# Kernel optimization log

Hardware: AMD Instinct MI355X
Metric: run time of the kernel (lower is better)

## Reference

```python
import jax, jax.numpy as jnp
import numpy as np

BS, V, S, K = 4, 2048, 7, 10
CLASS_NUM, VEC_NUM, CAT = 6, 8, 16
OUT_HEAD = CLASS_NUM + VEC_NUM * 3  # 30
DIM_FUSE = 128 + 128 + 256 + 256 + 512 + 512 + 16  # 1808


def _normalize(x, axis):
    return x / jnp.maximum(jnp.linalg.norm(x, axis=axis, keepdims=True), 1e-12)


def knn_index(verts, k):
    # verts: (b, v, 3) -> (b, v, k) excluding self
    inner = jnp.einsum('bnd,bmd->bnm', verts, verts)
    sq = jnp.sum(verts * verts, axis=2)
    dist = sq[:, :, None] + sq[:, None, :] - 2.0 * inner
    _, idx = jax.lax.top_k(-dist, k + 1)
    return idx[:, :, 1:]


def nearest_index(target, source):
    # target: (b, v1, 3), source: (b, v2, 3) -> (b, v1)
    inner = jnp.einsum('bnd,bmd->bnm', target, source)
    d = jnp.sum(source * source, 2)[:, None, :] + jnp.sum(target * target, 2)[:, :, None] - 2.0 * inner
    return jnp.argmin(d, axis=-1)


def gather_nb(t, idx):
    # t: (b, v, d), idx: (b, v1, k) -> (b, v1, k, d)
    return jax.vmap(lambda tt, ii: tt[ii])(t, idx)


def gather1(t, idx):
    # t: (b, v, d), idx: (b, v1) -> (b, v1, d)
    return jax.vmap(lambda tt, ii: tt[ii])(t, idx)


def bn_train(x, g, b, eps=1e-5):
    # x: (b, v, c); BatchNorm1d training-mode over (batch, vertices)
    m = jnp.mean(x, axis=(0, 1), keepdims=True)
    v = jnp.var(x, axis=(0, 1), keepdims=True)
    return (x - m) * jax.lax.rsqrt(v + eps) * g + b


def conv_surface(nb_idx, verts, directions, s, kernel_num):
    nd = _normalize(gather_nb(verts, nb_idx) - verts[:, :, None, :], -1)  # (b,v,n,3)
    sd = _normalize(directions, 0)  # (3, s*k)
    theta = jax.nn.relu(jnp.einsum('bvnd,dk->bvnk', nd, sd))
    b_, v_, n_, _ = theta.shape
    theta = theta.reshape(b_, v_, n_, s, kernel_num)
    return jnp.sum(jnp.max(theta, axis=2), axis=2)  # (b, v, kernel_num)


def conv_layer(nb_idx, verts, fm, w, b, directions, s, out_ch):
    nd = _normalize(gather_nb(verts, nb_idx) - verts[:, :, None, :], -1)
    sd = _normalize(directions, 0)  # (3, s*out_ch)
    theta = jax.nn.relu(jnp.einsum('bvnd,dk->bvnk', nd, sd))  # (b,v,n,s*o)
    fo = jnp.einsum('bvc,ck->bvk', fm, w) + b  # (b, v, (s+1)*o)
    center = fo[..., :out_ch]
    supp = gather_nb(fo[..., out_ch:], nb_idx)  # (b,v,n,s*o)
    act = (theta * supp).reshape(theta.shape[0], theta.shape[1], theta.shape[2], s, out_ch)
    act = jnp.sum(jnp.max(act, axis=2), axis=2)  # (b, v, o)
    return center + act


def pool_layer(verts, fm, pooling_rate, nb_num):
    idx = knn_index(verts, nb_num)
    pooled = jnp.max(gather_nb(fm, idx), axis=2)
    pool_num = verts.shape[1] // pooling_rate
    # deterministic subsample (torch uses randperm; fixed arange for reproducibility)
    return verts[:, :pool_num], pooled[:, :pool_num]


def setup_inputs() -> dict:
    key = jax.random.key(0)
    ks = jax.random.split(key, 16)
    def rn(i, shape, scale=0.05):
        return jax.random.normal(ks[i], shape, dtype=jnp.float32) * scale
    z = lambda *s: jnp.zeros(s, jnp.float32)
    o = lambda *s: jnp.ones(s, jnp.float32)
    return {
        'vertices': jax.random.normal(ks[0], (BS, V, 3), dtype=jnp.float32),
        'onehot': jax.nn.one_hot(jax.random.randint(ks[1], (BS,), 0, CAT), CAT, dtype=jnp.float32),
        'dir0': rn(2, (3, S * 128)),
        'w1': rn(3, (128, (S + 1) * 128)), 'b1': z((S + 1) * 128), 'dir1': rn(4, (3, S * 128)),
        'w2': rn(5, (128, (S + 1) * 256)), 'b2': z((S + 1) * 256), 'dir2': rn(6, (3, S * 256)),
        'w3': rn(7, (256, (S + 1) * 256)), 'b3': z((S + 1) * 256), 'dir3': rn(8, (3, S * 256)),
        'w4': rn(9, (256, (S + 1) * 512)), 'b4': z((S + 1) * 512), 'dir4': rn(10, (3, S * 512)),
        'g_bn1': o(128), 'be_bn1': z(128),
        'g_bn2': o(256), 'be_bn2': z(256),
        'g_bn3': o(256), 'be_bn3': z(256),
        'wc1': rn(11, (512, DIM_FUSE)), 'bc1': z(512),
        'wc2': rn(12, (512, 512)), 'bc2': z(512),
        'wc3': rn(13, (OUT_HEAD, 512)), 'bc3': z(OUT_HEAD),
    }


def reference(vertices, onehot, dir0, w1, b1, dir1, w2, b2, dir2, w3, b3, dir3,
              w4, b4, dir4, g_bn1, be_bn1, g_bn2, be_bn2, g_bn3, be_bn3,
              wc1, bc1, wc2, bc2, wc3, bc3):
    bs, v_num, _ = vertices.shape
    nb = knn_index(vertices, K)
    fm0 = jax.nn.relu(conv_surface(nb, vertices, dir0, S, 128))
    fm1 = jax.nn.relu(bn_train(conv_layer(nb, vertices, fm0, w1, b1, dir1, S, 128), g_bn1, be_bn1))
    vp1, fp1 = pool_layer(vertices, fm1, 4, 4)
    nb1 = knn_index(vp1, min(K, vp1.shape[1] // 8))
    fm2 = jax.nn.relu(bn_train(conv_layer(nb1, vp1, fp1, w2, b2, dir2, S, 256), g_bn2, be_bn2))
    fm3 = jax.nn.relu(bn_train(conv_layer(nb1, vp1, fm2, w3, b3, dir3, S, 256), g_bn3, be_bn3))
    vp2, fp2 = pool_layer(vp1, fm3, 4, 4)
    nb2 = knn_index(vp2, min(K, vp2.shape[1] // 8))
    fm4 = conv_layer(nb2, vp2, fp2, w4, b4, dir4, S, 512)
    f_global = jnp.max(fm4, axis=1)  # (b, 512)
    n1 = nearest_index(vertices, vp1)
    n2 = nearest_index(vertices, vp2)
    fm2u = gather1(fm2, n1)
    fm3u = gather1(fm3, n1)
    fm4u = gather1(fm4, n2)
    fg = jnp.broadcast_to(f_global[:, None, :], (bs, v_num, 512))
    oh = jnp.broadcast_to(onehot[:, None, :], (bs, v_num, CAT))
    feat = jnp.concatenate([fm0, fm1, fm2u, fm3u, fm4u, oh], axis=2)
    fuse = jnp.concatenate([fm0, fm1, fm2u, fm3u, fm4u, fg, oh], axis=2)
    h = jax.nn.relu(jnp.einsum('bvc,oc->bvo', fuse, wc1) + bc1)
    h = jax.nn.relu(jnp.einsum('bvc,oc->bvo', h, wc2) + bc2)
    pred = jnp.einsum('bvc,oc->bvo', h, wc3) + bc3
    seg = pred[..., :CLASS_NUM]
    vecs = pred[..., CLASS_NUM:CLASS_NUM + VEC_NUM * 3]
    return (seg, vecs, feat)
```

## Files before the change

kernel.cpp:

```cpp
#include <hip/hip_runtime.h>
#include <hip/hip_bf16.h>
#include <math.h>

#define BSZ 4
#define VN 2048
#define SS 7
#define KNB 10

typedef __attribute__((ext_vector_type(8))) short short8;
typedef __attribute__((ext_vector_type(4))) float f32x4;
typedef __attribute__((address_space(1))) const void gcvoid;
typedef __attribute__((address_space(3))) void lvoid;

__device__ inline ushort f2bf(float x) {
    __hip_bfloat16 h = __float2bfloat16(x);
    return *(ushort*)&h;
}

__device__ inline void gl2lds16(const ushort* g, ushort* l) {
    __builtin_amdgcn_global_load_lds((gcvoid*)g, (lvoid*)l, 16, 0, 0);
}

__device__ inline unsigned fenc(float f) {
    unsigned b = __float_as_uint(f);
    return (b & 0x80000000u) ? ~b : (b | 0x80000000u);
}
__device__ inline float fdec(unsigned e) {
    unsigned b = (e & 0x80000000u) ? (e & 0x7FFFFFFFu) : ~e;
    return __uint_as_float(b);
}

#define INS(dq, iq, dd, jj) { bool lt_ = (dd) < (dq); \
    float dmn_ = lt_ ? (dd) : (dq); float dmx_ = lt_ ? (dq) : (dd); \
    int imn_ = lt_ ? (jj) : (iq); int imx_ = lt_ ? (iq) : (jj); \
    (dq) = dmn_; (iq) = imn_; (dd) = dmx_; (jj) = imx_; }

#define PB0 8960L
#define PB1 24320L
#define PB2 958208L
#define PB3 1220352L

__global__ void prep_uber(const float* __restrict__ d0, const float* __restrict__ d1,
                          const float* __restrict__ d2, const float* __restrict__ d3,
                          const float* __restrict__ d4,
                          float* __restrict__ s0, float* __restrict__ s1,
                          float* __restrict__ s2, float* __restrict__ s3, float* __restrict__ s4,
                          const float* __restrict__ wc3, float* __restrict__ wc3t,
                          const float* __restrict__ wc1, ushort* __restrict__ wc1b,
                          const float* __restrict__ wc2, ushort* __restrict__ wc2b) {
    long i = blockIdx.x * 256L + threadIdx.x;
    if (i < PB0) {
        const float* src; float* dst; int C, c;
        if (i < 896)        { src = d0; dst = s0; C = 896;  c = (int)i; }
        else if (i < 1792)  { src = d1; dst = s1; C = 896;  c = (int)i - 896; }
        else if (i < 3584)  { src = d2; dst = s2; C = 1792; c = (int)i - 1792; }
        else if (i < 5376)  { src = d3; dst = s3; C = 1792; c = (int)i - 3584; }
        else                { src = d4; dst = s4; C = 3584; c = (int)i - 5376; }
        float a = src[c], b = src[C + c], e = src[2 * C + c];
        float den = fmaxf(sqrtf(a * a + b * b + e * e), 1e-12f);
        dst[c] = a / den; dst[C + c] = b / den; dst[2 * C + c] = e / den;
    } else if (i < PB1) {
        long j = i - PB0;
        int o = (int)(j / 512), k = (int)(j % 512);
        wc3t[(long)k * 30 + o] = wc3[j];
    } else if (i < PB2) {
        long j = i - PB1;
        int c = (int)(j % 1824);
        long r = j / 1824;
        wc1b[j] = f2bf(c < 1808 ? wc1[r * 1808 + c] : 0.f);
    } else if (i < PB3) {
        long j = i - PB2;
        wc2b[j] = f2bf(wc2[j]);
    }
}

__global__ __launch_bounds__(256) void wt_trans_all(const float* __restrict__ w1, const float* __restrict__ w2,
                                                    const float* __restrict__ w3, const float* __restrict__ w4,
                                                    ushort* __restrict__ o1, ushort* __restrict__ o2,
                                                    ushort* __restrict__ o3, ushort* __restrict__ o4) {
    __shared__ float tile[32][33];
    int gb = blockIdx.x;
    const float* w; ushort* o; int K, N, t;
    if (gb < 128)      { w = w1; o = o1; K = 128; N = 1024; t = gb; }
    else if (gb < 384) { w = w2; o = o2; K = 128; N = 2048; t = gb - 128; }
    else if (gb < 896) { w = w3; o = o3; K = 256; N = 2048; t = gb - 384; }
    else               { w = w4; o = o4; K = 256; N = 4096; t = gb - 896; }
    int tn = t % (N / 32), tk = t / (N / 32);
    int n0 = tn * 32, k0 = tk * 32;
    int tx = threadIdx.x % 32, ty = threadIdx.x / 32;
#pragma unroll
    for (int r = 0; r < 32; r += 8)
        tile[ty + r][tx] = w[(long)(k0 + ty + r) * N + n0 + tx];
    __syncthreads();
#pragma unroll
    for (int r = 0; r < 32; r += 8)
        o[(long)(n0 + ty + r) * K + k0 + tx] = f2bf(tile[tx][ty + r]);
}

#define KOFF0 0L
#define KOFF1 2621440L
#define KOFF2 2785280L
#define KTOT  2795520L

__device__ void knn_part_dev(const float* __restrict__ verts, int T, int nch,
                             int tile, int b, int ch,
                             float* __restrict__ pd, int* __restrict__ pi,
                             float4* __restrict__ s4) {
    const float* vb = verts + (long)b * VN * 3;
    int j0 = ch * 128;
    for (int j = threadIdx.x; j < 128; j += 128) {
        float x = vb[(j0 + j) * 3 + 0];
        float y = vb[(j0 + j) * 3 + 1];
        float z = vb[(j0 + j) * 3 + 2];
        s4[j] = make_float4(x, y, z, x * x + y * y + z * z);
    }
    __syncthreads();
    int i = tile * 128 + (int)threadIdx.x;
    if (i >= T) return;
    float px = vb[i * 3], py = vb[i * 3 + 1], pz = vb[i * 3 + 2];
    float d0[10], d1[10]; int id0[10], id1[10];
#pragma unroll
    for (int q = 0; q < 10; q++) { d0[q] = 1e30f; id0[q] = 0; d1[q] = 1e30f; id1[q] = 0; }
    for (int j = 0; j < 64; j++) {
        float4 sA = s4[j];
        float4 sB = s4[64 + j];
        float dA = fmaf(-2.f, px * sA.x + py * sA.y + pz * sA.z, sA.w);
        float dB = fmaf(-2.f, px * sB.x + py * sB.y + pz * sB.z, sB.w);
        int jA = j0 + j, jB = j0 + 64 + j;
        dA = (jA == i) ? 1e30f : dA;
        dB = (jB == i) ? 1e30f : dB;
#pragma unroll
        for (int q = 0; q < 10; q++) { INS(d0[q], id0[q], dA, jA); }
#pragma unroll
        for (int q = 0; q < 10; q++) { INS(d1[q], id1[q], dB, jB); }
    }
    long base = (((long)b * T + i) * nch * 2 + 2 * ch) * 10;
#pragma unroll
    for (int q = 0; q < 10; q++) { pd[base + q] = d0[q]; pi[base + q] = id0[q]; }
#pragma unroll
    for (int q = 0; q < 10; q++) { pd[base + 10 + q] = d1[q]; pi[base + 10 + q] = id1[q]; }
}

__device__ void nearest_dev(const float* __restrict__ verts, int SN, int* __restrict__ out,
                            int gl, float4* __restrict__ s4) {
    int t = gl * 128 + (int)threadIdx.x;
    int b = t / VN;
    const float* vb = verts + (long)b * VN * 3;
    for (int j = threadIdx.x; j < SN; j += 128) {
        float x = vb[j * 3], y = vb[j * 3 + 1], z = vb[j * 3 + 2];
        s4[j] = make_float4(x, y, z, x * x + y * y + z * z);
    }
    __syncthreads();
    int i = t % VN;
    float px = vb[i * 3], py = vb[i * 3 + 1], pz = vb[i * 3 + 2];
    int h = SN / 2;
    float b0 = 1e30f, b1 = 1e30f; int i0 = 0, i1 = 0;
    for (int j = 0; j < h; j++) {
        float4 sA = s4[j];
        float4 sB = s4[h + j];
        float dA = fmaf(-2.f, px * sA.x + py * sA.y + pz * sA.z, sA.w);
        float dB = fmaf(-2.f, px * sB.x + py * sB.y + pz * sB.z, sB.w);
        bool lA = dA < b0; b0 = lA ? dA : b0; i0 = lA ? j : i0;
        bool lB = dB < b1; b1 = lB ? dB : b1; i1 = lB ? (h + j) : i1;
    }
    out[t] = (b1 < b0) ? i1 : i0;
}

__global__ __launch_bounds__(128) void knn_part_uber(const float* __restrict__ verts,
                                                     float* __restrict__ pd, int* __restrict__ pi,
                                                     int* __restrict__ n1, int* __restrict__ n2) {
    __shared__ float4 smem[512];
    int gb = blockIdx.x;
    if (gb < 1024) {
        int tile = gb & 15, bc = gb >> 4;
        knn_part_dev(verts, 2048, 16, tile, bc >> 4, bc & 15, pd + KOFF0, pi + KOFF0, smem);
    } else if (gb < 1088) {
        int local = gb - 1024;
        int tile = local & 3, bc = local >> 2;
        knn_part_dev(verts, 512, 4, tile, bc >> 2, bc & 3, pd + KOFF1, pi + KOFF1, smem);
    } else if (gb < 1092) {
        int local = gb - 1088;
        knn_part_dev(verts, 128, 1, 0, local, 0, pd + KOFF2, pi + KOFF2, smem);
    } else if (gb < 1156) {
        nearest_dev(verts, 512, n1, gb - 1092, smem);
    } else {
        nearest_dev(verts, 128, n2, gb - 1156, smem);
    }
}

template <int NCH>
__device__ void knn_merge_dev(const float* __restrict__ pd, const int* __restrict__ pi,
                              int blk, int Tb,
                              int* __restrict__ out, int* __restrict__ outp, int Tp,
                              float* sdl, int* sil) {
    int tgt = threadIdx.x >> 2;
    int sub = threadIdx.x & 3;
    long t = (long)blk * 64 + tgt;
    constexpr int GRP = (NCH + 3) / 4;
    float d[10]; int id[10];
#pragma unroll
    for (int q = 0; q < 10; q++) { d[q] = 1e30f; id[q] = 0; }
    int c0 = sub * GRP;
    int c1 = (c0 + GRP < NCH) ? c0 + GRP : NCH;
    for (int c = c0; c < c1; c++) {
        long base = (t * NCH + c) * 10;
        for (int q = 0; q < 10; q++) {
            float dd = pd[base + q];
            if (dd >= d[9]) break;
            int jj = pi[base + q];
#pragma unroll
            for (int p = 0; p < 10; p++) { INS(d[p], id[p], dd, jj); }
        }
    }
    float* md = sdl + (tgt * 4 + sub) * 10;
    int* mi = sil + (tgt * 4 + sub) * 10;
#pragma unroll
    for (int q = 0; q < 10; q++) { md[q] = d[q]; mi[q] = id[q]; }
    __syncthreads();
    if (sub == 0) {
        for (int s = 1; s < 4; s++) {
            const float* od = sdl + (tgt * 4 + s) * 10;
            const int* oi = sil + (tgt * 4 + s) * 10;
            for (int q = 0; q < 10; q++) {
                float dd = od[q];
                if (dd >= d[9]) break;
                int jj = oi[q];
#pragma unroll
                for (int p = 0; p < 10; p++) { INS(d[p], id[p], dd, jj); }
            }
        }
#pragma unroll
        for (int q = 0; q < 10; q++) out[t * 10 + q] = id[q];
        if (outp) {
            int b = (int)(t / Tb), i = (int)(t % Tb);
            if (i < Tp) {
#pragma unroll
                for (int q = 0; q < 4; q++)
                    outp[((long)b * Tp + i) * 4 + q] = id[q];
            }
        }
    }
}

__global__ __launch_bounds__(256) void knn_merge_uber(const float* __restrict__ pd, const int* __restrict__ pi,
                                                      int* __restrict__ nb, int* __restrict__ nb1,
                                                      int* __restrict__ nb2, int* __restrict__ nbp1,
                                                      int* __restrict__ nbp2) {
    __shared__ float sdl[64 * 4 * 10];
    __shared__ int   sil[64 * 4 * 10];
    int gb = blockIdx.x;
    if (gb < 128)      knn_merge_dev<32>(pd + KOFF0, pi + KOFF0, gb, 2048, nb, nbp1, 512, sdl, sil);
    else if (gb < 160) knn_merge_dev<8>(pd + KOFF1, pi + KOFF1, gb - 128, 512, nb1, nbp2, 128, sdl, sil);
    else               knn_merge_dev<2>(pd + KOFF2, pi + KOFF2, gb - 160, 128, nb2, nullptr, 1, sdl, sil);
}

__global__ void conv_surface_kernel(const float* __restrict__ verts, const int* __restrict__ nb,
                                    const float* __restrict__ sd, float* __restrict__ fm0,
                                    ushort* __restrict__ fm0b) {
    int bv = blockIdx.x;
    int b = bv / VN, v = bv % VN;
    __shared__ float snd[KNB][3];
    int tid = threadIdx.x;
    if (tid < KNB) {
        int nj = nb[(long)bv * KNB + tid];
        const float* vb = verts + (long)b * VN * 3;
        float dx = vb[nj * 3] - vb[v * 3];
        float dy = vb[nj * 3 + 1] - vb[v * 3 + 1];
        float dz = vb[nj * 3 + 2] - vb[v * 3 + 2];
        float den = fmaxf(sqrtf(dx * dx + dy * dy + dz * dz), 1e-12f);
        snd[tid][0] = dx / den; snd[tid][1] = dy / den; snd[tid][2] = dz / den;
    }
    __syncthreads();
    int c = tid;
    float acc = 0.f;
    for (int s = 0; s < SS; s++) {
        int col = s * 128 + c;
        float s0 = sd[col], s1 = sd[896 + col], s2 = sd[2 * 896 + col];
        float m = 0.f;
#pragma unroll
        for (int n = 0; n < KNB; n++) {
            float dot = snd[n][0] * s0 + snd[n][1] * s1 + snd[n][2] * s2;
            m = fmaxf(m, dot);
        }
        acc += m;
    }
    fm0[(long)bv * 128 + c] = acc;
    fm0b[(long)bv * 128 + c] = f2bf(acc);
}

__global__ void conv_act_kernel(const float* __restrict__ verts, const int* __restrict__ nb,
                                const float* __restrict__ sd, const float* __restrict__ fo,
                                float* __restrict__ out, unsigned* __restrict__ fgmax,
                                int Vl, int outC) {
    int bv = blockIdx.x;
    int b = bv / Vl, v = bv % Vl;
    __shared__ float snd[KNB][3];
    __shared__ int srow[KNB];
    int tid = threadIdx.x;
    if (tid < KNB) {
        int nj = nb[(long)bv * KNB + tid];
        srow[tid] = b * Vl + nj;
        const float* vb = verts + (long)b * VN * 3;
        float dx = vb[nj * 3] - vb[v * 3];
        float dy = vb[nj * 3 + 1] - vb[v * 3 + 1];
        float dz = vb[nj * 3 + 2] - vb[v * 3 + 2];
        float den = fmaxf(sqrtf(dx * dx + dy * dy + dz * dz), 1e-12f);
        snd[tid][0] = dx / den; snd[tid][1] = dy / den; snd[tid][2] = dz / den;
    }
    __syncthreads();
    int c = tid;
    int SC = SS * outC;
    int foN = SC + outC;
    float acc = fo[(long)bv * foN + c];
    for (int s = 0; s < SS; s++) {
        int col = s * outC + c;
        float s0 = sd[col], s1 = sd[SC + col], s2 = sd[2 * SC + col];
        float m = -1e30f;
#pragma unroll
        for (int n = 0; n < KNB; n++) {
            float dot = snd[n][0] * s0 + snd[n][1] * s1 + snd[n][2] * s2;
            float th = fmaxf(dot, 0.f);
            float sup = fo[(long)srow[n] * foN + outC + col];
            m = fmaxf(m, th * sup);
        }
        acc += m;
    }
    out[(long)bv * outC + c] = acc;
    if (fgmax) atomicMax(&fgmax[b * outC + c], fenc(acc));
}

__global__ __launch_bounds__(256) void bn_stat_kernel(const float* __restrict__ x,
                                                      float* __restrict__ stat, int R, int C) {
    int rp = 256 / C;
    int c = threadIdx.x % C;
    int rs = threadIdx.x / C;
    float s = 0.f, s2 = 0.f;
    for (long r = (long)blockIdx.x * rp + rs; r < R; r += (long)gridDim.x * rp) {
        float v = x[r * C + c];
        s += v; s2 += v * v;
    }
    atomicAdd(&stat[c], s);
    atomicAdd(&stat[C + c], s2);
}

__global__ void bn_apply_relu_kernel(const float* __restrict__ x, const float* __restrict__ stat,
                                     const float* __restrict__ g, const float* __restrict__ be,
                                     float* __restrict__ out, ushort* __restrict__ outb, int R, int C) {
    long i = blockIdx.x * 256L + threadIdx.x;
    if (i >= (long)R * C) return;
    int c = (int)(i % C);
    float mu = stat[c] / R;
    float var = stat[C + c] / R - mu * mu;
    var = fmaxf(var, 0.f);
    float y = (x[i] - mu) * rsqrtf(var + 1e-5f) * g[c] + be[c];
    y = fmaxf(y, 0.f);
    out[i] = y;
    if (outb) outb[i] = f2bf(y);
}

__global__ void pool_b_kernel(const float* __restrict__ fm, const int* __restrict__ idx,
                              ushort* __restrict__ out, int Vin, int T, int C) {
    long i = blockIdx.x * 256L + threadIdx.x;
    if (i >= (long)BSZ * T * C) return;
    int c = (int)(i % C);
    long bt = i / C;
    int b = (int)(bt / T), t = (int)(bt % T);
    const int* id = idx + ((long)b * T + t) * 4;
    float m = -1e30f;
#pragma unroll
    for (int n = 0; n < 4; n++)
        m = fmaxf(m, fm[((long)b * Vin + id[n]) * C + c]);
    out[i] = f2bf(m);
}

__global__ __launch_bounds__(256) void gemm_mfma_bt_kernel(
    const ushort* __restrict__ A, const ushort* __restrict__ Bt,
    const float* __restrict__ bias, float* __restrict__ Cf, ushort* __restrict__ Cb,
    int M, int N, int K, int relu)
{
    __shared__ ushort As[128 * 32];
    __shared__ ushort Bs[128 * 32];
    int t = threadIdx.x;
    int w = t >> 6, l = t & 63;
    int quad = l >> 4, lm = l & 15;
    int wm = w >> 1, wn = w & 1;
    long m0 = blockIdx.y * 128L;
    long n0 = blockIdx.x * 128L;
    int lr = t >> 2;
    int lk = (t & 3) * 8;
    f32x4 acc[4][4];
#pragma unroll
    for (int i = 0; i < 4; i++)
#pragma unroll
        for (int j = 0; j < 4; j++) acc[i][j] = (f32x4){0.f, 0.f, 0.f, 0.f};

    for (int k0 = 0; k0 < K; k0 += 32) {
        __syncthreads();
        gl2lds16(A + (m0 + lr) * K + k0 + lk, &As[lr * 32 + lk]);
        gl2lds16(A + (m0 + 64 + lr) * K + k0 + lk, &As[(64 + lr) * 32 + lk]);
        gl2lds16(Bt + (n0 + lr) * K + k0 + lk, &Bs[lr * 32 + lk]);
        gl2lds16(Bt + (n0 + 64 + lr) * K + k0 + lk, &Bs[(64 + lr) * 32 + lk]);
        __syncthreads();
        short8 af[4], bfr[4];
#pragma unroll
        for (int i = 0; i < 4; i++)
            af[i] = *(const short8*)&As[(wm * 64 + i * 16 + lm) * 32 + quad * 8];
#pragma unroll
        for (int j = 0; j < 4; j++)
            bfr[j] = *(const short8*)&Bs[(wn * 64 + j * 16 + lm) * 32 + quad * 8];
#pragma unroll
        for (int i = 0; i < 4; i++)
#pragma unroll
            for (int j = 0; j < 4; j++)
                acc[i][j] = __builtin_amdgcn_mfma_f32_16x16x32_bf16(af[i], bfr[j], acc[i][j], 0, 0, 0);
    }
#pragma unroll
    for (int i = 0; i < 4; i++) {
#pragma unroll
        for (int j = 0; j < 4; j++) {
            int n = (int)n0 + wn * 64 + j * 16 + lm;
            float bv = bias[n];
#pragma unroll
            for (int r = 0; r < 4; r++) {
                int m = (int)m0 + wm * 64 + i * 16 + quad * 4 + r;
                float v = acc[i][j][r] + bv;
                if (relu) v = fmaxf(v, 0.f);
                if (Cf) Cf[(long)m * N + n] = v;
                if (Cb) Cb[(long)m * N + n] = f2bf(v);
            }
        }
    }
}

__global__ __launch_bounds__(256) void gemm_mfma_bt64_kernel(
    const ushort* __restrict__ A, const ushort* __restrict__ Bt,
    const float* __restrict__ bias, float* __restrict__ Cf, ushort* __restrict__ Cb,
    int M, int N, int K, int relu)
{
    __shared__ ushort As[64 * 32];
    __shared__ ushort Bs[128 * 32];
    int t = threadIdx.x;
    int w = t >> 6, l = t & 63;
    int quad = l >> 4, lm = l & 15;
    int wm = w >> 1, wn = w & 1;
    long m0 = blockIdx.y * 64L;
    long n0 = blockIdx.x * 128L;
    int lr = t >> 2;
    int lk = (t & 3) * 8;
    f32x4 acc[2][4];
#pragma unroll
    for (int i = 0; i < 2; i++)
#pragma unroll
        for (int j = 0; j < 4; j++) acc[i][j] = (f32x4){0.f, 0.f, 0.f, 0.f};

    for (int k0 = 0; k0 < K; k0 += 32) {
        __syncthreads();
        gl2lds16(A + (m0 + lr) * K + k0 + lk, &As[lr * 32 + lk]);
        gl2lds16(Bt + (n0 + lr) * K + k0 + lk, &Bs[lr * 32 + lk]);
        gl2lds16(Bt + (n0 + 64 + lr) * K + k0 + lk, &Bs[(64 + lr) * 32 + lk]);
        __syncthreads();
        short8 af[2], bfr[4];
#pragma unroll
        for (int i = 0; i < 2; i++)
            af[i] = *(const short8*)&As[(wm * 32 + i * 16 + lm) * 32 + quad * 8];
#pragma unroll
        for (int j = 0; j < 4; j++)
            bfr[j] = *(const short8*)&Bs[(wn * 64 + j * 16 + lm) * 32 + quad * 8];
#pragma unroll
        for (int i = 0; i < 2; i++)
#pragma unroll
            for (int j = 0; j < 4; j++)
                acc[i][j] = __builtin_amdgcn_mfma_f32_16x16x32_bf16(af[i], bfr[j], acc[i][j], 0, 0, 0);
    }
#pragma unroll
    for (int i = 0; i < 2; i++) {
#pragma unroll
        for (int j = 0; j < 4; j++) {
            int n = (int)n0 + wn * 64 + j * 16 + lm;
            float bv = bias[n];
#pragma unroll
            for (int r = 0; r < 4; r++) {
                int m = (int)m0 + wm * 32 + i * 16 + quad * 4 + r;
                float v = acc[i][j][r] + bv;
                if (relu) v = fmaxf(v, 0.f);
                if (Cf) Cf[(long)m * N + n] = v;
                if (Cb) Cb[(long)m * N + n] = f2bf(v);
            }
        }
    }
}

__global__ __launch_bounds__(256) void wc3_kernel(const float* __restrict__ h2,
                                                  const float* __restrict__ wc3t,
                                                  const float* __restrict__ bc3,
                                                  float* __restrict__ out) {
    int r8 = threadIdx.x >> 5;
    int c = threadIdx.x & 31;
    long row = blockIdx.x * 8L + r8;
    const float* hr = h2 + row * 512;
    float acc = 0.f;
    if (c < 30) {
        for (int k = 0; k < 512; k++)
            acc += hr[k] * wc3t[k * 30 + c];
        acc += bc3[c];
        if (c < 6) out[row * 6 + c] = acc;
        else       out[49152 + row * 24 + (c - 6)] = acc;
    }
}

__global__ __launch_bounds__(256) void fuse_bf_kernel(
    const float* __restrict__ fm0, const float* __restrict__ fm1,
    const float* __restrict__ fm2, const float* __restrict__ fm3,
    const float* __restrict__ fm4, const unsigned* __restrict__ fg_enc,
    const float* __restrict__ onehot,
    const int* __restrict__ n1, const int* __restrict__ n2,
    ushort* __restrict__ fuse_b, float* __restrict__ feat) {
    long row = blockIdx.x;
    int b = (int)(row >> 11);
    int i1 = n1[row], i2 = n2[row];
    const float* p0 = fm0 + row * 128;
    const float* p1 = fm1 + row * 128;
    const float* p2 = fm2 + ((long)b * 512 + i1) * 256;
    const float* p3 = fm3 + ((long)b * 512 + i1) * 256;
    const float* p4 = fm4 + ((long)b * 128 + i2) * 512;
    const unsigned* pg = fg_enc + b * 512;
    const float* po = onehot + b * 16;
    ushort* fb = fuse_b + row * 1824;
    float* ft = feat + row * 1296;
#pragma unroll
    for (int k = 0; k < 8; k++) {
        int c = threadIdx.x + k * 256;
        if (c >= 1824) break;
        float val = 0.f;
        if (c < 128)       val = p0[c];
        else if (c < 256)  val = p1[c - 128];
        else if (c < 512)  val = p2[c - 256];
        else if (c < 768)  val = p3[c - 512];
        else if (c < 1280) val = p4[c - 768];
        else if (c < 1792) val = fdec(pg[c - 1280]);
        else if (c < 1808) val = po[c - 1792];
        fb[c] = f2bf(val);
        if (c < 1280)                   ft[c] = val;
        else if (c >= 1792 && c < 1808) ft[c - 512] = val;
    }
}


extern "C" void kernel_launch(void* const* d_in, const int* in_sizes, int n_in,
                              void* d_out, int out_size, void* d_ws, size_t ws_size,
                              hipStream_t stream) {
    const float* verts  = (const float*)d_in[0];
    const float* onehot = (const float*)d_in[1];
    const float* dir0 = (const float*)d_in[2];
    const float* w1 = (const float*)d_in[3];
    const float* b1 = (const float*)d_in[4];
    const float* dir1 = (const float*)d_in[5];
    const float* w2 = (const float*)d_in[6];
    const float* b2 = (const float*)d_in[7];
    const float* dir2 = (const float*)d_in[8];
    const float* w3 = (const float*)d_in[9];
    const float* b3 = (const float*)d_in[10];
    const float* dir3 = (const float*)d_in[11];
    const float* w4 = (const float*)d_in[12];
    const float* b4 = (const float*)d_in[13];
    const float* dir4 = (const float*)d_in[14];
    const float* g_bn1 = (const float*)d_in[15];
    const float* be_bn1 = (const float*)d_in[16];
    const float* g_bn2 = (const float*)d_in[17];
    const float* be_bn2 = (const float*)d_in[18];
    const float* g_bn3 = (const float*)d_in[19];
    const float* be_bn3 = (const float*)d_in[20];
    const float* wc1 = (const float*)d_in[21];
    const float* bc1 = (const float*)d_in[22];
    const float* wc2 = (const float*)d_in[23];
    const float* bc2 = (const float*)d_in[24];
    const float* wc3 = (const float*)d_in[25];
    const float* bc3 = (const float*)d_in[26];
    float* outf = (float*)d_out;

    float* wsf = (float*)d_ws;
    size_t off = 0;
    auto alloc = [&](size_t n) { float* p = wsf + off; off += (n + 15) & ~(size_t)15; return p; };

    float* sd0 = alloc(3 * 896);
    float* sd1 = alloc(3 * 896);
    float* sd2 = alloc(3 * 1792);
    float* sd3 = alloc(3 * 1792);
    float* sd4 = alloc(3 * 3584);
    float* wc3t = alloc(512L * 30);
    float* fm0 = alloc(8192L * 128);
    float* fm1 = alloc(8192L * 128);
    float* c1  = alloc(8192L * 128);
    float* fm2 = alloc(2048L * 256);
    float* c2  = alloc(2048L * 256);
    float* fm3 = alloc(2048L * 256);
    float* c3  = alloc(2048L * 256);
    float* fm4 = alloc(512L * 512);
    float* statbase = alloc(3328);
    float* stat1 = statbase;
    float* stat2 = statbase + 256;
    float* stat3 = statbase + 768;
    unsigned* fg_enc = (unsigned*)(statbase + 1280);
    float* fbuf = alloc(8192L * 1024);
    float* h2 = alloc(8192L * 512);
    float* pd  = alloc(KTOT);
    int* pi    = (int*)alloc(KTOT);
    int* nb   = (int*)alloc(8192L * KNB);
    int* nb1  = (int*)alloc(2048L * KNB);
    int* nb2  = (int*)alloc(512L * KNB);
    int* nbp1 = (int*)alloc(2048L * 4);
    int* nbp2 = (int*)alloc(512L * 4);
    int* n1   = (int*)alloc(8192);
    int* n2   = (int*)alloc(8192);
    ushort* fuse_b = (ushort*)alloc(8192L * 1824 / 2);
    ushort* h1b    = (ushort*)alloc(8192L * 512 / 2);
    ushort* wc1b   = (ushort*)alloc(512L * 1824 / 2);
    ushort* wc2b   = (ushort*)alloc(512L * 512 / 2);
    ushort* w1tb   = (ushort*)alloc(1024L * 128 / 2);
    ushort* w2tb   = (ushort*)alloc(2048L * 128 / 2);
    ushort* w3tb   = (ushort*)alloc(2048L * 256 / 2);
    ushort* w4tb   = (ushort*)alloc(4096L * 256 / 2);
    ushort* fm0b   = (ushort*)alloc(8192L * 128 / 2);
    ushort* fp1b   = (ushort*)alloc(2048L * 128 / 2);
    ushort* fm2b   = (ushort*)alloc(2048L * 256 / 2);
    ushort* fp2b   = (ushort*)alloc(512L * 256 / 2);

    auto nblk = [](long n, int b) { return (unsigned)((n + b - 1) / b); };

    hipMemsetAsync(statbase, 0, 3328 * sizeof(float), stream);
    prep_uber<<<nblk(PB3, 256), 256, 0, stream>>>(dir0, dir1, dir2, dir3, dir4,
                                                  sd0, sd1, sd2, sd3, sd4,
                                                  wc3, wc3t, wc1, wc1b, wc2, wc2b);
    wt_trans_all<<<1920, 256, 0, stream>>>(w1, w2, w3, w4, w1tb, w2tb, w3tb, w4tb);

    knn_part_uber<<<1220, 128, 0, stream>>>(verts, pd, pi, n1, n2);
    knn_merge_uber<<<168, 256, 0, stream>>>(pd, pi, nb, nb1, nb2, nbp1, nbp2);

    conv_surface_kernel<<<BSZ * 2048, 128, 0, stream>>>(verts, nb, sd0, fm0, fm0b);

    gemm_mfma_bt_kernel<<<dim3(8, 64), 256, 0, stream>>>(fm0b, w1tb, b1, fbuf, nullptr, 8192, 1024, 128, 0);
    conv_act_kernel<<<BSZ * 2048, 128, 0, stream>>>(verts, nb, sd1, fbuf, c1, nullptr, 2048, 128);
    bn_stat_kernel<<<256, 256, 0, stream>>>(c1, stat1, 8192, 128);
    bn_apply_relu_kernel<<<nblk(8192L * 128, 256), 256, 0, stream>>>(c1, stat1, g_bn1, be_bn1, fm1, nullptr, 8192, 128);

    pool_b_kernel<<<nblk(BSZ * 512L * 128, 256), 256, 0, stream>>>(fm1, nbp1, fp1b, 2048, 512, 128);

    gemm_mfma_bt64_kernel<<<dim3(16, 32), 256, 0, stream>>>(fp1b, w2tb, b2, fbuf, nullptr, 2048, 2048, 128, 0);
    conv_act_kernel<<<BSZ * 512, 256, 0, stream>>>(verts, nb1, sd2, fbuf, c2, nullptr, 512, 256);
    bn_stat_kernel<<<256, 256, 0, stream>>>(c2, stat2, 2048, 256);
    bn_apply_relu_kernel<<<nblk(2048L * 256, 256), 256, 0, stream>>>(c2, stat2, g_bn2, be_bn2, fm2, fm2b, 2048, 256);

    gemm_mfma_bt64_kernel<<<dim3(16, 32), 256, 0, stream>>>(fm2b, w3tb, b3, fbuf, nullptr, 2048, 2048, 256, 0);
    conv_act_kernel<<<BSZ * 512, 256, 0, stream>>>(verts, nb1, sd3, fbuf, c3, nullptr, 512, 256);
    bn_stat_kernel<<<256, 256, 0, stream>>>(c3, stat3, 2048, 256);
    bn_apply_relu_kernel<<<nblk(2048L * 256, 256), 256, 0, stream>>>(c3, stat3, g_bn3, be_bn3, fm3, nullptr, 2048, 256);

    pool_b_kernel<<<nblk(BSZ * 128L * 256, 256), 256, 0, stream>>>(fm3, nbp2, fp2b, 512, 128, 256);

    gemm_mfma_bt64_kernel<<<dim3(32, 8), 256, 0, stream>>>(fp2b, w4tb, b4, fbuf, nullptr, 512, 4096, 256, 0);
    conv_act_kernel<<<BSZ * 128, 512, 0, stream>>>(verts, nb2, sd4, fbuf, fm4, fg_enc, 128, 512);

    fuse_bf_kernel<<<8192, 256, 0, stream>>>(fm0, fm1, fm2, fm3, fm4, fg_enc, onehot,
                                             n1, n2, fuse_b, outf + 245760);

    gemm_mfma_bt64_kernel<<<dim3(4, 128), 256, 0, stream>>>(fuse_b, wc1b, bc1, nullptr, h1b, 8192, 512, 1824, 1);
    gemm_mfma_bt64_kernel<<<dim3(4, 128), 256, 0, stream>>>(h1b, wc2b, bc2, h2, nullptr, 8192, 512, 512, 1);
    wc3_kernel<<<1024, 256, 0, stream>>>(h2, wc3t, bc3, outf);
}
```

Before: 490.2 us.

## Split KNN candidate chunks into four partial lists and widen merge parallelism

The partial KNN kernel now runs 256 threads per block, one query each, and keeps four independent top-10 lists per query, one per 32-candidate slice, instead of two. That gives more independent insertion chains per thread for instruction-level parallelism. Partial indices are stored as ushort to offset the doubled partial-list volume. The merge kernel uses 8 sub-threads per target over 64/16/4 lists. In exchange it raises register pressure, doubles the partial distance traffic and adds more merge work.

```diff
diff --git a/kernel.cpp b/kernel.cpp
--- a/kernel.cpp
+++ b/kernel.cpp
@@ -98,55 +98,73 @@
 }
 
 #define KOFF0 0L
-#define KOFF1 2621440L
-#define KOFF2 2785280L
-#define KTOT  2795520L
+#define KOFF1 5242880L
+#define KOFF2 5570560L
+#define KTOT  5591040L
 
 __device__ void knn_part_dev(const float* __restrict__ verts, int T, int nch,
                              int tile, int b, int ch,
-                             float* __restrict__ pd, int* __restrict__ pi,
+                             float* __restrict__ pd, ushort* __restrict__ pi,
                              float4* __restrict__ s4) {
     const float* vb = verts + (long)b * VN * 3;
     int j0 = ch * 128;
-    for (int j = threadIdx.x; j < 128; j += 128) {
+    for (int j = threadIdx.x; j < 128; j += 256) {
         float x = vb[(j0 + j) * 3 + 0];
         float y = vb[(j0 + j) * 3 + 1];
         float z = vb[(j0 + j) * 3 + 2];
         s4[j] = make_float4(x, y, z, x * x + y * y + z * z);
     }
     __syncthreads();
-    int i = tile * 128 + (int)threadIdx.x;
+    int i = tile * 256 + (int)threadIdx.x;
     if (i >= T) return;
     float px = vb[i * 3], py = vb[i * 3 + 1], pz = vb[i * 3 + 2];
-    float d0[10], d1[10]; int id0[10], id1[10];
-#pragma unroll
-    for (int q = 0; q < 10; q++) { d0[q] = 1e30f; id0[q] = 0; d1[q] = 1e30f; id1[q] = 0; }
-    for (int j = 0; j < 64; j++) {
+    float d0[10], d1[10], d2[10], d3[10];
+    int id0[10], id1[10], id2[10], id3[10];
+#pragma unroll
+    for (int q = 0; q < 10; q++) {
+        d0[q] = 1e30f; d1[q] = 1e30f; d2[q] = 1e30f; d3[q] = 1e30f;
+        id0[q] = 0; id1[q] = 0; id2[q] = 0; id3[q] = 0;
+    }
+    for (int j = 0; j < 32; j++) {
         float4 sA = s4[j];
-        float4 sB = s4[64 + j];
+        float4 sB = s4[32 + j];
+        float4 sC = s4[64 + j];
+        float4 sD = s4[96 + j];
         float dA = fmaf(-2.f, px * sA.x + py * sA.y + pz * sA.z, sA.w);
         float dB = fmaf(-2.f, px * sB.x + py * sB.y + pz * sB.z, sB.w);
-        int jA = j0 + j, jB = j0 + 64 + j;
+        float dC = fmaf(-2.f, px * sC.x + py * sC.y + pz * sC.z, sC.w);
+        float dD = fmaf(-2.f, px * sD.x + py * sD.y + pz * sD.z, sD.w);
+        int jA = j0 + j, jB = j0 + 32 + j, jC = j0 + 64 + j, jD = j0 + 96 + j;
         dA = (jA == i) ? 1e30f : dA;
         dB = (jB == i) ? 1e30f : dB;
+        dC = (jC == i) ? 1e30f : dC;
+        dD = (jD == i) ? 1e30f : dD;
 #pragma unroll
         for (int q = 0; q < 10; q++) { INS(d0[q], id0[q], dA, jA); }
 #pragma unroll
         for (int q = 0; q < 10; q++) { INS(d1[q], id1[q], dB, jB); }
-    }
-    long base = (((long)b * T + i) * nch * 2 + 2 * ch) * 10;
-#pragma unroll
-    for (int q = 0; q < 10; q++) { pd[base + q] = d0[q]; pi[base + q] = id0[q]; }
-#pragma unroll
-    for (int q = 0; q < 10; q++) { pd[base + 10 + q] = d1[q]; pi[base + 10 + q] = id1[q]; }
+#pragma unroll
+        for (int q = 0; q < 10; q++) { INS(d2[q], id2[q], dC, jC); }
+#pragma unroll
+        for (int q = 0; q < 10; q++) { INS(d3[q], id3[q], dD, jD); }
+    }
+    long base = ((long)(b * T + i) * nch + ch) * 40;
+#pragma unroll
+    for (int q = 0; q < 10; q++) { pd[base + q] = d0[q];      pi[base + q] = (ushort)id0[q]; }
+#pragma unroll
+    for (int q = 0; q < 10; q++) { pd[base + 10 + q] = d1[q]; pi[base + 10 + q] = (ushort)id1[q]; }
+#pragma unroll
+    for (int q = 0; q < 10; q++) { pd[base + 20 + q] = d2[q]; pi[base + 20 + q] = (ushort)id2[q]; }
+#pragma unroll
+    for (int q = 0; q < 10; q++) { pd[base + 30 + q] = d3[q]; pi[base + 30 + q] = (ushort)id3[q]; }
 }
 
 __device__ void nearest_dev(const float* __restrict__ verts, int SN, int* __restrict__ out,
                             int gl, float4* __restrict__ s4) {
-    int t = gl * 128 + (int)threadIdx.x;
+    int t = gl * 256 + (int)threadIdx.x;
     int b = t / VN;
     const float* vb = verts + (long)b * VN * 3;
-    for (int j = threadIdx.x; j < SN; j += 128) {
+    for (int j = threadIdx.x; j < SN; j += 256) {
         float x = vb[j * 3], y = vb[j * 3 + 1], z = vb[j * 3 + 2];
         s4[j] = make_float4(x, y, z, x * x + y * y + z * z);
     }
@@ -166,61 +184,61 @@
     out[t] = (b1 < b0) ? i1 : i0;
 }
 
-__global__ __launch_bounds__(128) void knn_part_uber(const float* __restrict__ verts,
-                                                     float* __restrict__ pd, int* __restrict__ pi,
+__global__ __launch_bounds__(256) void knn_part_uber(const float* __restrict__ verts,
+                                                     float* __restrict__ pd, ushort* __restrict__ pi,
                                                      int* __restrict__ n1, int* __restrict__ n2) {
     __shared__ float4 smem[512];
     int gb = blockIdx.x;
-    if (gb < 1024) {
-        int tile = gb & 15, bc = gb >> 4;
+    if (gb < 512) {
+        int tile = gb & 7, bc = gb >> 3;
         knn_part_dev(verts, 2048, 16, tile, bc >> 4, bc & 15, pd + KOFF0, pi + KOFF0, smem);
-    } else if (gb < 1088) {
-        int local = gb - 1024;
-        int tile = local & 3, bc = local >> 2;
+    } else if (gb < 544) {
+        int local = gb - 512;
+        int tile = local & 1, bc = local >> 1;
         knn_part_dev(verts, 512, 4, tile, bc >> 2, bc & 3, pd + KOFF1, pi + KOFF1, smem);
-    } else if (gb < 1092) {
-        int local = gb - 1088;
+    } else if (gb < 548) {
+        int local = gb - 544;
         knn_part_dev(verts, 128, 1, 0, local, 0, pd + KOFF2, pi + KOFF2, smem);
-    } else if (gb < 1156) {
-        nearest_dev(verts, 512, n1, gb - 1092, smem);
+    } else if (gb < 580) {
+        nearest_dev(verts, 512, n1, gb - 548, smem);
     } else {
-        nearest_dev(verts, 128, n2, gb - 1156, smem);
-    }
-}
-
-template <int NCH>
-__device__ void knn_merge_dev(const float* __restrict__ pd, const int* __restrict__ pi,
+        nearest_dev(verts, 128, n2, gb - 580, smem);
+    }
+}
+
+template <int NL>
+__device__ void knn_merge_dev(const float* __restrict__ pd, const ushort* __restrict__ pi,
                               int blk, int Tb,
                               int* __restrict__ out, int* __restrict__ outp, int Tp,
                               float* sdl, int* sil) {
-    int tgt = threadIdx.x >> 2;
-    int sub = threadIdx.x & 3;
-    long t = (long)blk * 64 + tgt;
-    constexpr int GRP = (NCH + 3) / 4;
+    int tgt = threadIdx.x >> 3;
+    int sub = threadIdx.x & 7;
+    long t = (long)blk * 32 + tgt;
+    constexpr int GRP = (NL + 7) / 8;
     float d[10]; int id[10];
 #pragma unroll
     for (int q = 0; q < 10; q++) { d[q] = 1e30f; id[q] = 0; }
     int c0 = sub * GRP;
-    int c1 = (c0 + GRP < NCH) ? c0 + GRP : NCH;
+    int c1 = (c0 + GRP < NL) ? c0 + GRP : NL;
     for (int c = c0; c < c1; c++) {
-        long base = (t * NCH + c) * 10;
+        long base = (t * NL + c) * 10;
         for (int q = 0; q < 10; q++) {
             float dd = pd[base + q];
             if (dd >= d[9]) break;
-            int jj = pi[base + q];
+            int jj = (int)pi[base + q];
 #pragma unroll
             for (int p = 0; p < 10; p++) { INS(d[p], id[p], dd, jj); }
         }
     }
-    float* md = sdl + (tgt * 4 + sub) * 10;
-    int* mi = sil + (tgt * 4 + sub) * 10;
+    float* md = sdl + (tgt * 8 + sub) * 10;
+    int* mi = sil + (tgt * 8 + sub) * 10;
 #pragma unroll
     for (int q = 0; q < 10; q++) { md[q] = d[q]; mi[q] = id[q]; }
     __syncthreads();
     if (sub == 0) {
-        for (int s = 1; s < 4; s++) {
-            const float* od = sdl + (tgt * 4 + s) * 10;
-            const int* oi = sil + (tgt * 4 + s) * 10;
+        for (int s = 1; s < 8; s++) {
+            const float* od = sdl + (tgt * 8 + s) * 10;
+            const int* oi = sil + (tgt * 8 + s) * 10;
             for (int q = 0; q < 10; q++) {
                 float dd = od[q];
                 if (dd >= d[9]) break;
@@ -242,16 +260,16 @@
     }
 }
 
-__global__ __launch_bounds__(256) void knn_merge_uber(const float* __restrict__ pd, const int* __restrict__ pi,
+__global__ __launch_bounds__(256) void knn_merge_uber(const float* __restrict__ pd, const ushort* __restrict__ pi,
                                                       int* __restrict__ nb, int* __restrict__ nb1,
                                                       int* __restrict__ nb2, int* __restrict__ nbp1,
                                                       int* __restrict__ nbp2) {
-    __shared__ float sdl[64 * 4 * 10];
-    __shared__ int   sil[64 * 4 * 10];
+    __shared__ float sdl[32 * 8 * 10];
+    __shared__ int   sil[32 * 8 * 10];
     int gb = blockIdx.x;
-    if (gb < 128)      knn_merge_dev<32>(pd + KOFF0, pi + KOFF0, gb, 2048, nb, nbp1, 512, sdl, sil);
-    else if (gb < 160) knn_merge_dev<8>(pd + KOFF1, pi + KOFF1, gb - 128, 512, nb1, nbp2, 128, sdl, sil);
-    else               knn_merge_dev<2>(pd + KOFF2, pi + KOFF2, gb - 160, 128, nb2, nullptr, 1, sdl, sil);
+    if (gb < 256)      knn_merge_dev<64>(pd + KOFF0, pi + KOFF0, gb, 2048, nb, nbp1, 512, sdl, sil);
+    else if (gb < 320) knn_merge_dev<16>(pd + KOFF1, pi + KOFF1, gb - 256, 512, nb1, nbp2, 128, sdl, sil);
+    else               knn_merge_dev<4>(pd + KOFF2, pi + KOFF2, gb - 320, 128, nb2, nullptr, 1, sdl, sil);
 }
 
 __global__ void conv_surface_kernel(const float* __restrict__ verts, const int* __restrict__ nb,
@@ -604,7 +622,7 @@
     float* fbuf = alloc(8192L * 1024);
     float* h2 = alloc(8192L * 512);
     float* pd  = alloc(KTOT);
-    int* pi    = (int*)alloc(KTOT);
+    ushort* pi = (ushort*)alloc(KTOT / 2);
     int* nb   = (int*)alloc(8192L * KNB);
     int* nb1  = (int*)alloc(2048L * KNB);
     int* nb2  = (int*)alloc(512L * KNB);
@@ -633,8 +651,8 @@
                                                   wc3, wc3t, wc1, wc1b, wc2, wc2b);
     wt_trans_all<<<1920, 256, 0, stream>>>(w1, w2, w3, w4, w1tb, w2tb, w3tb, w4tb);
 
-    knn_part_uber<<<1220, 128, 0, stream>>>(verts, pd, pi, n1, n2);
-    knn_merge_uber<<<168, 256, 0, stream>>>(pd, pi, nb, nb1, nb2, nbp1, nbp2);
+    knn_part_uber<<<612, 256, 0, stream>>>(verts, pd, pi, n1, n2);
+    knn_merge_uber<<<336, 256, 0, stream>>>(pd, pi, nb, nb1, nb2, nbp1, nbp2);
 
     conv_surface_kernel<<<BSZ * 2048, 128, 0, stream>>>(verts, nb, sd0, fm0, fm0b);
 
```

Result: slower. 505.8 us (+3.2%).
